# Kernel optimization log

Hardware: AMD Instinct MI355X
Metric: run time of the kernel (lower is better)

Reference implementation:

```python
import jax, jax.numpy as jnp
import numpy as np

VOCAB, EDIM, WFEAT, LABELS, SLOPE = 50000, 128, 128, 2, 0.01
N = 8192

def setup_inputs() -> dict:
    key = jax.random.key(0)
    ks = jax.random.split(key, 8)
    inSen = jax.random.randint(ks[0], (N,), 0, VOCAB, dtype=jnp.int64) if jax.config.read('jax_enable_x64') else jax.random.randint(ks[0], (N,), 0, VOCAB, dtype=jnp.int32)
    adj = jax.random.randint(ks[1], (N, N), 0, 2, dtype=jnp.int32)
    emb = jax.random.normal(ks[2], (VOCAB, EDIM), dtype=jnp.float32)
    W = jax.random.normal(ks[3], (EDIM, WFEAT), dtype=jnp.float32) * (1.0 / np.sqrt(EDIM))
    a_src = jax.random.normal(ks[4], (WFEAT,), dtype=jnp.float32) * (1.0 / np.sqrt(WFEAT))
    a_dst = jax.random.normal(ks[5], (WFEAT,), dtype=jnp.float32) * (1.0 / np.sqrt(WFEAT))
    cls_W = jax.random.normal(ks[6], (WFEAT, LABELS), dtype=jnp.float32) * (1.0 / np.sqrt(WFEAT))
    cls_b = jax.random.normal(ks[7], (LABELS,), dtype=jnp.float32) * 0.01
    return {"inSen": inSen, "adj": adj, "selfLink": 1, "emb": emb, "W": W,
            "a_src": a_src, "a_dst": a_dst, "cls_W": cls_W, "cls_b": cls_b}

def reference(inSen, adj, selfLink, emb, W, a_src, a_dst, cls_W, cls_b):
    # Embedding lookup: (N, edim)
    words = emb[inSen]
    # GAT layer: linear projection then adjacency-masked additive attention
    h = words @ W                              # (N, wFeat)
    f_src = h @ a_src                          # (N,)
    f_dst = h @ a_dst                          # (N,)
    e = jax.nn.leaky_relu(f_src[:, None] + f_dst[None, :], negative_slope=SLOPE)  # (N, N)
    mask = (adj + selfLink * jnp.eye(adj.shape[0], dtype=adj.dtype)) > 0
    e = jnp.where(mask, e, jnp.float32(-1e9))
    attention = jax.nn.softmax(e, axis=1)      # (N, N)
    sentence = attention @ h                   # (N, wFeat)
    # Max pool over words, classify
    poolSentence = jnp.max(sentence, axis=0)   # (wFeat,)
    label = jax.nn.softmax(poolSentence @ cls_W + cls_b, axis=0)  # (labels,)
    return (poolSentence, attention, sentence, label)
```

## Files before the change

### kernel.cpp

```cpp
#include <hip/hip_runtime.h>
#include <hip/hip_bf16.h>

#define NR 8192
#define WF 128

typedef short bf16x8 __attribute__((ext_vector_type(8)));
typedef float f32x4 __attribute__((ext_vector_type(4)));

static __device__ __forceinline__ unsigned int f2bf(float f) {
    unsigned int u = __float_as_uint(f);
    return (u + 0x7fffu + ((u >> 16) & 1u)) >> 16;
}
static __device__ __forceinline__ void atomicMaxF(float* addr, float v) {
    if (v >= 0.f) atomicMax((int*)addr, __float_as_int(v));
    else          atomicMin((unsigned int*)addr, __float_as_uint(v));
}
static __device__ __forceinline__ float lrelu(float x) { return x > 0.f ? x : 0.01f * x; }

__global__ __launch_bounds__(256) void k_proj(
    const int* __restrict__ inSen, const float* __restrict__ emb,
    const float* __restrict__ W, const float* __restrict__ a_src,
    const float* __restrict__ a_dst, float* __restrict__ f_src,
    float* __restrict__ f_dst, unsigned short* __restrict__ hB)
{
    __shared__ float ht[16 * 132];
    const int t = threadIdx.x;
    const int f = t & 127, rh = t >> 7;
    const int i0 = blockIdx.x * 16;

    int wd[8];
    #pragma unroll
    for (int r = 0; r < 8; ++r) wd[r] = inSen[i0 + rh * 8 + r];
    float h[8];
    #pragma unroll
    for (int r = 0; r < 8; ++r) h[r] = 0.f;

    for (int k4 = 0; k4 < 32; ++k4) {
        const float w0 = W[(k4 * 4 + 0) * WF + f];
        const float w1 = W[(k4 * 4 + 1) * WF + f];
        const float w2 = W[(k4 * 4 + 2) * WF + f];
        const float w3 = W[(k4 * 4 + 3) * WF + f];
        #pragma unroll
        for (int r = 0; r < 8; ++r) {
            float4 ev = ((const float4*)(emb + (size_t)wd[r] * 128))[k4];
            h[r] += ev.x * w0 + ev.y * w1 + ev.z * w2 + ev.w * w3;
        }
    }
    #pragma unroll
    for (int r = 0; r < 8; ++r) ht[(rh * 8 + r) * 132 + f] = h[r];
    __syncthreads();

    if (t < 16) {
        float s = 0.f, d = 0.f;
        for (int k4 = 0; k4 < 32; ++k4) {
            float4 hv = *(const float4*)(ht + t * 132 + k4 * 4);
            float4 as = ((const float4*)a_src)[k4];
            float4 ad = ((const float4*)a_dst)[k4];
            s += hv.x * as.x + hv.y * as.y + hv.z * as.z + hv.w * as.w;
            d += hv.x * ad.x + hv.y * ad.y + hv.z * ad.z + hv.w * ad.w;
        }
        f_src[i0 + t] = s;
        f_dst[i0 + t] = d;
    }
    {
        const int kb = blockIdx.x >> 1, half = blockIdx.x & 1;
        const int nf = t >> 5, l32 = t & 31;
        const int qloc = l32 >> 4, fx = l32 & 15;
        const int lane = (half * 2 + qloc) * 16 + fx;
        const float* hp = ht + (qloc * 8) * 132 + nf * 16 + fx;
        uint4 v;
        v.x = f2bf(hp[0 * 132]) | (f2bf(hp[1 * 132]) << 16);
        v.y = f2bf(hp[2 * 132]) | (f2bf(hp[3 * 132]) << 16);
        v.z = f2bf(hp[4 * 132]) | (f2bf(hp[5 * 132]) << 16);
        v.w = f2bf(hp[6 * 132]) | (f2bf(hp[7 * 132]) << 16);
        *(uint4*)(hB + ((size_t)kb * 8 + nf) * 512 + lane * 8) = v;
    }
}

__global__ __launch_bounds__(256) void k_aux(
    const float* __restrict__ f_dst, float* __restrict__ maxfd, float* __restrict__ pool)
{
    __shared__ float s[256];
    const int t = threadIdx.x;
    float m = -1e30f;
    for (int j = t; j < NR; j += 256) m = fmaxf(m, f_dst[j]);
    s[t] = m;
    __syncthreads();
    for (int o = 128; o > 0; o >>= 1) {
        if (t < o) s[t] = fmaxf(s[t], s[t + o]);
        __syncthreads();
    }
    if (t == 0) maxfd[0] = s[0];
    if (t < WF) pool[t] = -INFINITY;
}

static __device__ __forceinline__ void adj_chunk(
    int c, int4 a, float4 f, int lane, int row, int sl,
    float fs, float C, int shl,
    unsigned int* __restrict__ mrow, float& sum)
{
    const bool m0 = a.x > 0, m1 = a.y > 0, m2 = a.z > 0, m3 = a.w > 0;
    float p0 = m0 ? __expf(lrelu(fs + f.x) - C) : 0.f;
    float p1 = m1 ? __expf(lrelu(fs + f.y) - C) : 0.f;
    float p2 = m2 ? __expf(lrelu(fs + f.z) - C) : 0.f;
    float p3 = m3 ? __expf(lrelu(fs + f.w) - C) : 0.f;
    unsigned int nib = (m0 ? 1u : 0u) | (m1 ? 2u : 0u) | (m2 ? 4u : 0u) | (m3 ? 8u : 0u);
    float ssum = p0 + p1 + p2 + p3;
    if (c == (row >> 8)) {
        if (lane == ((row & 255) >> 2)) {
            const int jd = row & 3;
            const int aj = jd == 0 ? a.x : jd == 1 ? a.y : jd == 2 ? a.z : a.w;
            const float fj = jd == 0 ? f.x : jd == 1 ? f.y : jd == 2 ? f.z : f.w;
            const bool mo = aj > 0, mn = (aj + sl) > 0;
            if (mn != mo) {
                const float pd = __expf(lrelu(fs + fj) - C);
                if (mn) { nib |= 1u << jd; ssum += pd; }
                else    { nib &= ~(1u << jd); ssum -= pd; }
            }
        }
    }
    sum += ssum;
    unsigned int v = nib << shl;
    v |= __shfl_xor(v, 1);
    v |= __shfl_xor(v, 2);
    v |= __shfl_xor(v, 4);
    if ((lane & 7) == 0) mrow[c * 8 + (lane >> 3)] = v;
}

__global__ __launch_bounds__(256, 4) void k_adj(
    const int* __restrict__ adj, const int* __restrict__ slP,
    const float* __restrict__ f_src, const float* __restrict__ f_dst,
    const float* __restrict__ maxfd, unsigned int* __restrict__ maskG,
    float* __restrict__ invl)
{
    const int t = threadIdx.x, lane = t & 63, w = t >> 6;
    const int row = blockIdx.x * 4 + w;
    const int sl = slP[0];
    const float fs = f_src[row];
    const float C = lrelu(fs + maxfd[0]);
    const int* __restrict__ ap = adj + (size_t)row * NR + 4 * lane;
    const float* __restrict__ fp = f_dst + 4 * lane;
    unsigned int* __restrict__ mrow = maskG + (size_t)row * 256;
    const int shl = 4 * (lane & 7);
    float sum = 0.f;

    int4   a0 = *(const int4*)(ap + 0 * 256);
    float4 f0 = *(const float4*)(fp + 0 * 256);
    int4   a1 = *(const int4*)(ap + 1 * 256);
    float4 f1 = *(const float4*)(fp + 1 * 256);

    for (int c = 0; c < 30; c += 2) {
        int4   a2 = *(const int4*)(ap + (c + 2) * 256);
        float4 f2 = *(const float4*)(fp + (c + 2) * 256);
        int4   a3 = *(const int4*)(ap + (c + 3) * 256);
        float4 f3 = *(const float4*)(fp + (c + 3) * 256);
        adj_chunk(c,     a0, f0, lane, row, sl, fs, C, shl, mrow, sum);
        adj_chunk(c + 1, a1, f1, lane, row, sl, fs, C, shl, mrow, sum);
        a0 = a2; f0 = f2; a1 = a3; f1 = f3;
    }
    adj_chunk(30, a0, f0, lane, row, sl, fs, C, shl, mrow, sum);
    adj_chunk(31, a1, f1, lane, row, sl, fs, C, shl, mrow, sum);

    #pragma unroll
    for (int o = 1; o < 64; o <<= 1) sum += __shfl_xor(sum, o);
    if (lane == 0) invl[row] = 1.0f / sum;
}

__global__ __launch_bounds__(256, 4) void k_att(
    const unsigned int* __restrict__ maskG, const float* __restrict__ f_src,
    const float* __restrict__ f_dst, const float* __restrict__ maxfd,
    const float* __restrict__ invl, const unsigned short* __restrict__ hB,
    float* __restrict__ att, float* __restrict__ sent)
{
    __shared__ float red[4][2048];
    const int t = threadIdx.x;
    const int lane = t & 63, w = t >> 6;
    const int gw = blockIdx.x * 4 + w;
    const int strip = gw >> 3, ks = gw & 7;
    const int i0 = strip * 16;
    const int fx = lane & 15, quad = lane >> 4;
    const int row = i0 + fx;
    const float fs = f_src[row];
    const float C = lrelu(fs + maxfd[0]);
    const float il = invl[row];
    float* __restrict__ ar = att + (size_t)row * NR;
    const unsigned int* __restrict__ mrow = maskG + (size_t)row * 256;
    f32x4 acc[8] = {};
    const int k0 = ks * 1024;

    for (int kk = k0; kk < k0 + 1024; kk += 32) {
        const int kb = kk >> 5;
        const unsigned short* hp = hB + (size_t)kb * 4096 + lane * 8;
        bf16x8 bfr[8];
        #pragma unroll
        for (int nf = 0; nf < 8; ++nf) bfr[nf] = *(const bf16x8*)(hp + nf * 512);

        const unsigned int mbyte = (mrow[kb] >> (quad * 8)) & 0xffu;
        const float4 fd0 = *(const float4*)(f_dst + kk + quad * 8);
        const float4 fd1 = *(const float4*)(f_dst + kk + quad * 8 + 4);
        const float fv[8] = {fd0.x, fd0.y, fd0.z, fd0.w, fd1.x, fd1.y, fd1.z, fd1.w};
        float p[8];
        #pragma unroll
        for (int j = 0; j < 8; ++j)
            p[j] = ((mbyte >> j) & 1u) ? __expf(lrelu(fs + fv[j]) - C) : 0.f;

        const float4 w0 = make_float4(p[0] * il, p[1] * il, p[2] * il, p[3] * il);
        const float4 w1 = make_float4(p[4] * il, p[5] * il, p[6] * il, p[7] * il);
        *(float4*)(ar + kk + quad * 8) = w0;
        *(float4*)(ar + kk + quad * 8 + 4) = w1;

        union { uint4 u; bf16x8 v; } cv;
        cv.u.x = f2bf(p[0]) | (f2bf(p[1]) << 16);
        cv.u.y = f2bf(p[2]) | (f2bf(p[3]) << 16);
        cv.u.z = f2bf(p[4]) | (f2bf(p[5]) << 16);
        cv.u.w = f2bf(p[6]) | (f2bf(p[7]) << 16);
        #pragma unroll
        for (int nf = 0; nf < 8; ++nf)
            acc[nf] = __builtin_amdgcn_mfma_f32_16x16x32_bf16(cv.v, bfr[nf], acc[nf], 0, 0, 0);
    }
    #pragma unroll
    for (int reg = 0; reg < 4; ++reg) {
        #pragma unroll
        for (int nf = 0; nf < 8; ++nf)
            red[w][(quad * 4 + reg) * 128 + nf * 16 + fx] = acc[nf][reg];
    }
    __syncthreads();
    {
        const int e0 = t * 8;
        const int m = e0 >> 7, f0 = e0 & 127;
        const float vin = invl[i0 + m];
        float* sp = sent + (size_t)(i0 + m) * WF + f0;
        #pragma unroll
        for (int j = 0; j < 8; ++j) {
            const float v = red[0][e0 + j] + red[1][e0 + j] + red[2][e0 + j] + red[3][e0 + j];
            atomicAdd(sp + j, v * vin);
        }
    }
}

__global__ __launch_bounds__(256) void k_pool(
    const float* __restrict__ sent, float* __restrict__ pool)
{
    __shared__ float s[256];
    const int t = threadIdx.x;
    const int f = t & 127, rh = t >> 7;
    const int r0 = blockIdx.x * 128;
    float m = -1e30f;
    for (int j = 0; j < 64; ++j)
        m = fmaxf(m, sent[(size_t)(r0 + j * 2 + rh) * WF + f]);
    s[t] = m;
    __syncthreads();
    if (t < 128) atomicMaxF(&pool[f], fmaxf(s[t], s[t + 128]));
}

__global__ __launch_bounds__(128) void k_label(
    const float* __restrict__ pool, const float* __restrict__ cls_W,
    const float* __restrict__ cls_b, float* __restrict__ label)
{
    __shared__ float s0[128], s1[128];
    const int t = threadIdx.x;
    float v = pool[t];
    s0[t] = v * cls_W[t * 2 + 0];
    s1[t] = v * cls_W[t * 2 + 1];
    __syncthreads();
    if (t == 0) {
        float z0 = cls_b[0], z1 = cls_b[1];
        for (int f = 0; f < 128; ++f) { z0 += s0[f]; z1 += s1[f]; }
        float m = fmaxf(z0, z1);
        float e0 = __expf(z0 - m), e1 = __expf(z1 - m);
        float inv = 1.0f / (e0 + e1);
        label[0] = e0 * inv;
        label[1] = e1 * inv;
    }
}

extern "C" void kernel_launch(void* const* d_in, const int* in_sizes, int n_in,
                              void* d_out, int out_size, void* d_ws, size_t ws_size,
                              hipStream_t stream)
{
    const int*   inSen    = (const int*)d_in[0];
    const int*   adj      = (const int*)d_in[1];
    const int*   selfLink = (const int*)d_in[2];
    const float* emb      = (const float*)d_in[3];
    const float* W        = (const float*)d_in[4];
    const float* a_src    = (const float*)d_in[5];
    const float* a_dst    = (const float*)d_in[6];
    const float* cls_W    = (const float*)d_in[7];
    const float* cls_b    = (const float*)d_in[8];

    float* out   = (float*)d_out;
    float* pool  = out;
    float* att   = out + 128;
    float* sent  = att + (size_t)NR * NR;
    float* label = sent + (size_t)NR * WF;

    char* ws = (char*)d_ws;
    unsigned short* hB    = (unsigned short*)ws;
    unsigned int*   maskG = (unsigned int*)(ws + (2u << 20));
    float* f_src = (float*)(ws + (10u << 20));
    float* f_dst = f_src + NR;
    float* invl  = f_dst + NR;
    float* maxfd = invl + NR;

    hipMemsetAsync(sent, 0, (size_t)NR * WF * sizeof(float), stream);
    k_proj<<<NR / 16, 256, 0, stream>>>(inSen, emb, W, a_src, a_dst, f_src, f_dst, hB);
    k_aux<<<1, 256, 0, stream>>>(f_dst, maxfd, pool);
    k_adj<<<NR / 4, 256, 0, stream>>>(adj, selfLink, f_src, f_dst, maxfd, maskG, invl);
    k_att<<<NR / 16 * 8 / 4, 256, 0, stream>>>(maskG, f_src, f_dst, maxfd, invl, hB, att, sent);
    k_pool<<<NR / 128, 256, 0, stream>>>(sent, pool);
    k_label<<<1, 128, 0, stream>>>(pool, cls_W, cls_b, label);
}
```

Measured before the change: 635.6 us.

## Fuse max reduction into projection, drop atomics in attention and pooling

Computes the f_dst max inside k_proj with a shuffle reduction and an atomic max, which removes the single-block k_aux kernel. k_att now gives each 16-row strip to one 512-thread block whose eight waves cover the full K range, so sentence rows are written with plain float4 stores instead of atomicAdd, and the memset of sent is no longer needed. k_adj prefetches four chunks ahead instead of two, mask words are loaded as uint4, and pooling writes per-block partials that k_label reduces without atomics. The memset of maxfd to 0xFF yields a negative NaN bit pattern, which the signed-int atomicMax path is meant to overwrite. Larger blocks with 64KB of shared memory may reduce occupancy.

```diff
diff --git a/kernel.cpp b/kernel.cpp
--- a/kernel.cpp
+++ b/kernel.cpp
@@ -21,7 +21,8 @@
     const int* __restrict__ inSen, const float* __restrict__ emb,
     const float* __restrict__ W, const float* __restrict__ a_src,
     const float* __restrict__ a_dst, float* __restrict__ f_src,
-    float* __restrict__ f_dst, unsigned short* __restrict__ hB)
+    float* __restrict__ f_dst, float* __restrict__ maxfd,
+    unsigned short* __restrict__ hB)
 {
     __shared__ float ht[16 * 132];
     const int t = threadIdx.x;
@@ -61,6 +62,10 @@
         }
         f_src[i0 + t] = s;
         f_dst[i0 + t] = d;
+        float dm = d;
+        #pragma unroll
+        for (int o = 1; o < 16; o <<= 1) dm = fmaxf(dm, __shfl_xor(dm, o));
+        if (t == 0) atomicMaxF(maxfd, dm);
     }
     {
         const int kb = blockIdx.x >> 1, half = blockIdx.x & 1;
@@ -75,23 +80,6 @@
         v.w = f2bf(hp[6 * 132]) | (f2bf(hp[7 * 132]) << 16);
         *(uint4*)(hB + ((size_t)kb * 8 + nf) * 512 + lane * 8) = v;
     }
-}
-
-__global__ __launch_bounds__(256) void k_aux(
-    const float* __restrict__ f_dst, float* __restrict__ maxfd, float* __restrict__ pool)
-{
-    __shared__ float s[256];
-    const int t = threadIdx.x;
-    float m = -1e30f;
-    for (int j = t; j < NR; j += 256) m = fmaxf(m, f_dst[j]);
-    s[t] = m;
-    __syncthreads();
-    for (int o = 128; o > 0; o >>= 1) {
-        if (t < o) s[t] = fmaxf(s[t], s[t + o]);
-        __syncthreads();
-    }
-    if (t == 0) maxfd[0] = s[0];
-    if (t < WF) pool[t] = -INFINITY;
 }
 
 static __device__ __forceinline__ void adj_chunk(
@@ -148,35 +136,48 @@
     float4 f0 = *(const float4*)(fp + 0 * 256);
     int4   a1 = *(const int4*)(ap + 1 * 256);
     float4 f1 = *(const float4*)(fp + 1 * 256);
-
-    for (int c = 0; c < 30; c += 2) {
-        int4   a2 = *(const int4*)(ap + (c + 2) * 256);
-        float4 f2 = *(const float4*)(fp + (c + 2) * 256);
-        int4   a3 = *(const int4*)(ap + (c + 3) * 256);
-        float4 f3 = *(const float4*)(fp + (c + 3) * 256);
-        adj_chunk(c,     a0, f0, lane, row, sl, fs, C, shl, mrow, sum);
+    int4   a2 = *(const int4*)(ap + 2 * 256);
+    float4 f2 = *(const float4*)(fp + 2 * 256);
+    int4   a3 = *(const int4*)(ap + 3 * 256);
+    float4 f3 = *(const float4*)(fp + 3 * 256);
+
+    #pragma unroll 1
+    for (int c = 0; c < 28; c += 4) {
+        int4   n0 = *(const int4*)(ap + (c + 4) * 256);
+        float4 g0 = *(const float4*)(fp + (c + 4) * 256);
+        int4   n1 = *(const int4*)(ap + (c + 5) * 256);
+        float4 g1 = *(const float4*)(fp + (c + 5) * 256);
+        int4   n2 = *(const int4*)(ap + (c + 6) * 256);
+        float4 g2 = *(const float4*)(fp + (c + 6) * 256);
+        int4   n3 = *(const int4*)(ap + (c + 7) * 256);
+        float4 g3 = *(const float4*)(fp + (c + 7) * 256);
+        adj_chunk(c + 0, a0, f0, lane, row, sl, fs, C, shl, mrow, sum);
         adj_chunk(c + 1, a1, f1, lane, row, sl, fs, C, shl, mrow, sum);
-        a0 = a2; f0 = f2; a1 = a3; f1 = f3;
-    }
-    adj_chunk(30, a0, f0, lane, row, sl, fs, C, shl, mrow, sum);
-    adj_chunk(31, a1, f1, lane, row, sl, fs, C, shl, mrow, sum);
+        adj_chunk(c + 2, a2, f2, lane, row, sl, fs, C, shl, mrow, sum);
+        adj_chunk(c + 3, a3, f3, lane, row, sl, fs, C, shl, mrow, sum);
+        a0 = n0; f0 = g0; a1 = n1; f1 = g1;
+        a2 = n2; f2 = g2; a3 = n3; f3 = g3;
+    }
+    adj_chunk(28, a0, f0, lane, row, sl, fs, C, shl, mrow, sum);
+    adj_chunk(29, a1, f1, lane, row, sl, fs, C, shl, mrow, sum);
+    adj_chunk(30, a2, f2, lane, row, sl, fs, C, shl, mrow, sum);
+    adj_chunk(31, a3, f3, lane, row, sl, fs, C, shl, mrow, sum);
 
     #pragma unroll
     for (int o = 1; o < 64; o <<= 1) sum += __shfl_xor(sum, o);
     if (lane == 0) invl[row] = 1.0f / sum;
 }
 
-__global__ __launch_bounds__(256, 4) void k_att(
+__global__ __launch_bounds__(512, 4) void k_att(
     const unsigned int* __restrict__ maskG, const float* __restrict__ f_src,
     const float* __restrict__ f_dst, const float* __restrict__ maxfd,
     const float* __restrict__ invl, const unsigned short* __restrict__ hB,
     float* __restrict__ att, float* __restrict__ sent)
 {
-    __shared__ float red[4][2048];
+    __shared__ float red[8][2048];
     const int t = threadIdx.x;
     const int lane = t & 63, w = t >> 6;
-    const int gw = blockIdx.x * 4 + w;
-    const int strip = gw >> 3, ks = gw & 7;
+    const int strip = blockIdx.x;
     const int i0 = strip * 16;
     const int fx = lane & 15, quad = lane >> 4;
     const int row = i0 + fx;
@@ -186,37 +187,43 @@
     float* __restrict__ ar = att + (size_t)row * NR;
     const unsigned int* __restrict__ mrow = maskG + (size_t)row * 256;
     f32x4 acc[8] = {};
-    const int k0 = ks * 1024;
-
-    for (int kk = k0; kk < k0 + 1024; kk += 32) {
-        const int kb = kk >> 5;
-        const unsigned short* hp = hB + (size_t)kb * 4096 + lane * 8;
-        bf16x8 bfr[8];
-        #pragma unroll
-        for (int nf = 0; nf < 8; ++nf) bfr[nf] = *(const bf16x8*)(hp + nf * 512);
-
-        const unsigned int mbyte = (mrow[kb] >> (quad * 8)) & 0xffu;
-        const float4 fd0 = *(const float4*)(f_dst + kk + quad * 8);
-        const float4 fd1 = *(const float4*)(f_dst + kk + quad * 8 + 4);
-        const float fv[8] = {fd0.x, fd0.y, fd0.z, fd0.w, fd1.x, fd1.y, fd1.z, fd1.w};
-        float p[8];
-        #pragma unroll
-        for (int j = 0; j < 8; ++j)
-            p[j] = ((mbyte >> j) & 1u) ? __expf(lrelu(fs + fv[j]) - C) : 0.f;
-
-        const float4 w0 = make_float4(p[0] * il, p[1] * il, p[2] * il, p[3] * il);
-        const float4 w1 = make_float4(p[4] * il, p[5] * il, p[6] * il, p[7] * il);
-        *(float4*)(ar + kk + quad * 8) = w0;
-        *(float4*)(ar + kk + quad * 8 + 4) = w1;
-
-        union { uint4 u; bf16x8 v; } cv;
-        cv.u.x = f2bf(p[0]) | (f2bf(p[1]) << 16);
-        cv.u.y = f2bf(p[2]) | (f2bf(p[3]) << 16);
-        cv.u.z = f2bf(p[4]) | (f2bf(p[5]) << 16);
-        cv.u.w = f2bf(p[6]) | (f2bf(p[7]) << 16);
-        #pragma unroll
-        for (int nf = 0; nf < 8; ++nf)
-            acc[nf] = __builtin_amdgcn_mfma_f32_16x16x32_bf16(cv.v, bfr[nf], acc[nf], 0, 0, 0);
+    const int k0 = w * 1024;
+
+    for (int kk4 = k0; kk4 < k0 + 1024; kk4 += 128) {
+        const uint4 mw = *(const uint4*)(mrow + (kk4 >> 5));
+        const unsigned int mwa[4] = {mw.x, mw.y, mw.z, mw.w};
+        #pragma unroll
+        for (int j4 = 0; j4 < 4; ++j4) {
+            const int kk = kk4 + j4 * 32;
+            const int kb = kk >> 5;
+            const unsigned short* hp = hB + (size_t)kb * 4096 + lane * 8;
+            bf16x8 bfr[8];
+            #pragma unroll
+            for (int nf = 0; nf < 8; ++nf) bfr[nf] = *(const bf16x8*)(hp + nf * 512);
+
+            const unsigned int mbyte = (mwa[j4] >> (quad * 8)) & 0xffu;
+            const float4 fd0 = *(const float4*)(f_dst + kk + quad * 8);
+            const float4 fd1 = *(const float4*)(f_dst + kk + quad * 8 + 4);
+            const float fv[8] = {fd0.x, fd0.y, fd0.z, fd0.w, fd1.x, fd1.y, fd1.z, fd1.w};
+            float p[8];
+            #pragma unroll
+            for (int j = 0; j < 8; ++j)
+                p[j] = ((mbyte >> j) & 1u) ? __expf(lrelu(fs + fv[j]) - C) : 0.f;
+
+            const float4 w0 = make_float4(p[0] * il, p[1] * il, p[2] * il, p[3] * il);
+            const float4 w1 = make_float4(p[4] * il, p[5] * il, p[6] * il, p[7] * il);
+            *(float4*)(ar + kk + quad * 8) = w0;
+            *(float4*)(ar + kk + quad * 8 + 4) = w1;
+
+            union { uint4 u; bf16x8 v; } cv;
+            cv.u.x = f2bf(p[0]) | (f2bf(p[1]) << 16);
+            cv.u.y = f2bf(p[2]) | (f2bf(p[3]) << 16);
+            cv.u.z = f2bf(p[4]) | (f2bf(p[5]) << 16);
+            cv.u.w = f2bf(p[6]) | (f2bf(p[7]) << 16);
+            #pragma unroll
+            for (int nf = 0; nf < 8; ++nf)
+                acc[nf] = __builtin_amdgcn_mfma_f32_16x16x32_bf16(cv.v, bfr[nf], acc[nf], 0, 0, 0);
+        }
     }
     #pragma unroll
     for (int reg = 0; reg < 4; ++reg) {
@@ -226,20 +233,23 @@
     }
     __syncthreads();
     {
-        const int e0 = t * 8;
+        const int e0 = t * 4;
         const int m = e0 >> 7, f0 = e0 & 127;
         const float vin = invl[i0 + m];
-        float* sp = sent + (size_t)(i0 + m) * WF + f0;
-        #pragma unroll
-        for (int j = 0; j < 8; ++j) {
-            const float v = red[0][e0 + j] + red[1][e0 + j] + red[2][e0 + j] + red[3][e0 + j];
-            atomicAdd(sp + j, v * vin);
-        }
+        float vv[4];
+        #pragma unroll
+        for (int j = 0; j < 4; ++j) {
+            float s = 0.f;
+            #pragma unroll
+            for (int sx = 0; sx < 8; ++sx) s += red[sx][e0 + j];
+            vv[j] = s * vin;
+        }
+        *(float4*)(sent + (size_t)(i0 + m) * WF + f0) = make_float4(vv[0], vv[1], vv[2], vv[3]);
     }
 }
 
 __global__ __launch_bounds__(256) void k_pool(
-    const float* __restrict__ sent, float* __restrict__ pool)
+    const float* __restrict__ sent, float* __restrict__ partial)
 {
     __shared__ float s[256];
     const int t = threadIdx.x;
@@ -250,24 +260,27 @@
         m = fmaxf(m, sent[(size_t)(r0 + j * 2 + rh) * WF + f]);
     s[t] = m;
     __syncthreads();
-    if (t < 128) atomicMaxF(&pool[f], fmaxf(s[t], s[t + 128]));
+    if (t < 128) partial[blockIdx.x * 128 + t] = fmaxf(s[t], s[t + 128]);
 }
 
 __global__ __launch_bounds__(128) void k_label(
-    const float* __restrict__ pool, const float* __restrict__ cls_W,
-    const float* __restrict__ cls_b, float* __restrict__ label)
+    const float* __restrict__ partial, const float* __restrict__ cls_W,
+    const float* __restrict__ cls_b, float* __restrict__ pool,
+    float* __restrict__ label)
 {
     __shared__ float s0[128], s1[128];
     const int t = threadIdx.x;
-    float v = pool[t];
-    s0[t] = v * cls_W[t * 2 + 0];
-    s1[t] = v * cls_W[t * 2 + 1];
+    float m = -1e30f;
+    for (int b = 0; b < 64; ++b) m = fmaxf(m, partial[b * 128 + t]);
+    pool[t] = m;
+    s0[t] = m * cls_W[t * 2 + 0];
+    s1[t] = m * cls_W[t * 2 + 1];
     __syncthreads();
     if (t == 0) {
         float z0 = cls_b[0], z1 = cls_b[1];
         for (int f = 0; f < 128; ++f) { z0 += s0[f]; z1 += s1[f]; }
-        float m = fmaxf(z0, z1);
-        float e0 = __expf(z0 - m), e1 = __expf(z1 - m);
+        float mm = fmaxf(z0, z1);
+        float e0 = __expf(z0 - mm), e1 = __expf(z1 - mm);
         float inv = 1.0f / (e0 + e1);
         label[0] = e0 * inv;
         label[1] = e1 * inv;
@@ -297,16 +310,16 @@
     char* ws = (char*)d_ws;
     unsigned short* hB    = (unsigned short*)ws;
     unsigned int*   maskG = (unsigned int*)(ws + (2u << 20));
-    float* f_src = (float*)(ws + (10u << 20));
-    float* f_dst = f_src + NR;
-    float* invl  = f_dst + NR;
-    float* maxfd = invl + NR;
-
-    hipMemsetAsync(sent, 0, (size_t)NR * WF * sizeof(float), stream);
-    k_proj<<<NR / 16, 256, 0, stream>>>(inSen, emb, W, a_src, a_dst, f_src, f_dst, hB);
-    k_aux<<<1, 256, 0, stream>>>(f_dst, maxfd, pool);
+    float* f_src   = (float*)(ws + (10u << 20));
+    float* f_dst   = f_src + NR;
+    float* invl    = f_dst + NR;
+    float* maxfd   = invl + NR;
+    float* partial = maxfd + 64;
+
+    hipMemsetAsync(maxfd, 0xFF, 4, stream);
+    k_proj<<<NR / 16, 256, 0, stream>>>(inSen, emb, W, a_src, a_dst, f_src, f_dst, maxfd, hB);
     k_adj<<<NR / 4, 256, 0, stream>>>(adj, selfLink, f_src, f_dst, maxfd, maskG, invl);
-    k_att<<<NR / 16 * 8 / 4, 256, 0, stream>>>(maskG, f_src, f_dst, maxfd, invl, hB, att, sent);
-    k_pool<<<NR / 128, 256, 0, stream>>>(sent, pool);
-    k_label<<<1, 128, 0, stream>>>(pool, cls_W, cls_b, label);
-}
+    k_att<<<NR / 16, 512, 0, stream>>>(maskG, f_src, f_dst, maxfd, invl, hB, att, sent);
+    k_pool<<<NR / 128, 256, 0, stream>>>(sent, partial);
+    k_label<<<1, 128, 0, stream>>>(partial, cls_W, cls_b, pool, label);
+}
```

Result: faster. 613.1 us (-3.5%).
